# Performance work log

Measured on AMD Instinct MI355X. Metric: run time of the kernel, lower is better.

Reference implementation:

```python
import jax, jax.numpy as jnp
import numpy as np
from jax import lax

DG = 8  # deformable groups


def conv3(x, w, b):
    # 3x3 stride-1 SAME conv, NCHW/OIHW
    y = lax.conv_general_dilated(x, w, (1, 1), 'SAME',
                                 dimension_numbers=('NCHW', 'OIHW', 'NCHW'))
    return y + b[None, :, None, None]


def lrelu(x):
    return jnp.where(x >= 0, x, 0.1 * x)


def _mdcn(x, offset, mask, w, b, dg):
    """Modulated deformable conv v2: 3x3, stride 1, pad 1, dilation 1, groups 1.
    offset: [B, 2*dg*9, H, W] (first dg*9 = y offsets, second dg*9 = x offsets),
    mask:   [B, dg*9, H, W] (already sigmoided)."""
    B, C, H, W = x.shape
    kk = 9
    Cg = C // dg
    off = offset.reshape(B, 2, dg, kk, H, W)
    oy, ox = off[:, 0], off[:, 1]            # [B, dg, kk, H, W]
    m = mask.reshape(B, dg, kk, H, W)
    ky = (jnp.arange(kk) // 3 - 1).astype(x.dtype).reshape(1, 1, kk, 1, 1)
    kx = (jnp.arange(kk) % 3 - 1).astype(x.dtype).reshape(1, 1, kk, 1, 1)
    hg = jnp.arange(H, dtype=x.dtype).reshape(1, 1, 1, H, 1)
    wg = jnp.arange(W, dtype=x.dtype).reshape(1, 1, 1, 1, W)
    py = hg + ky + oy                        # sampling positions (pad=1 cancels k-1 shift)
    px = wg + kx + ox
    y0 = jnp.floor(py)
    x0 = jnp.floor(px)
    wy = py - y0
    wx = px - x0
    xg = x.reshape(B, dg, Cg, H * W)
    acc = jnp.zeros((B, dg, Cg, kk, H, W), x.dtype)
    for dy, dx, wgt in ((0.0, 0.0, (1 - wy) * (1 - wx)),
                        (0.0, 1.0, (1 - wy) * wx),
                        (1.0, 0.0, wy * (1 - wx)),
                        (1.0, 1.0, wy * wx)):
        yy = y0 + dy
        xx = x0 + dx
        valid = (yy >= 0) & (yy < H) & (xx >= 0) & (xx < W)
        yi = jnp.clip(yy, 0, H - 1).astype(jnp.int32)
        xi = jnp.clip(xx, 0, W - 1).astype(jnp.int32)
        idx = (yi * W + xi).reshape(B, dg, 1, kk * H * W)
        v = jnp.take_along_axis(xg, idx, axis=3).reshape(B, dg, Cg, kk, H, W)
        acc = acc + v * (wgt * valid.astype(x.dtype))[:, :, None]
    acc = acc * m[:, :, None]                # modulation mask
    sampled = acc.reshape(B, C, kk, H, W)
    out = jnp.einsum('bckhw,ock->bohw', sampled, w.reshape(w.shape[0], C, kk))
    return out + b[None, :, None, None]


def _dcn_pack(x, feat, w_om, b_om, w, b):
    out = conv3(feat, w_om, b_om)            # [B, 3*dg*9, H, W]
    o1, o2, mr = jnp.split(out, 3, axis=1)
    offset = jnp.concatenate([o1, o2], axis=1)
    mask = jax.nn.sigmoid(mr)
    return _mdcn(x, offset, mask, w, b, DG)


def _forward(ref, neb,
             w_oc1, b_oc1, w_om1, b_om1, w_dcn1, b_dcn1, w_fc, b_fc,
             w_cas1, b_cas1, w_cas2, b_cas2, w_om2, b_om2, w_dcn2, b_dcn2,
             w_ta1, b_ta1, w_ta2, b_ta2, w_ff, b_ff):
    start = ref
    # --- PCD alignment (nbr_feat_l = neb, ref_feat_l = ref) ---
    off = lrelu(conv3(jnp.concatenate([neb, ref], axis=1), w_oc1, b_oc1))
    feat = _dcn_pack(neb, off, w_om1, b_om1, w_dcn1, b_dcn1)
    feat = lrelu(conv3(feat, w_fc, b_fc))
    off = jnp.concatenate([feat, ref], axis=1)
    off = lrelu(conv3(lrelu(conv3(off, w_cas1, b_cas1)), w_cas2, b_cas2))
    feat = lrelu(_dcn_pack(feat, off, w_om2, b_om2, w_dcn2, b_dcn2))
    # --- TSA fusion (ref=ref, neb=feat) ---
    emb_ref = conv3(ref, w_ta1, b_ta1)
    emb = conv3(feat, w_ta2, b_ta2)
    corr = jnp.sum(emb * emb_ref, axis=1, keepdims=True)  # [B,1,H,W]
    feat = lrelu(conv3(ref * corr, w_ff, b_ff))
    return feat + start


def setup_inputs() -> dict:
    key = jax.random.key(0)
    ks = jax.random.split(key, 32)
    B, C, H, W = 4, 64, 180, 320
    s = 0.05
    p = lambda k, shape: (jax.random.normal(k, shape, jnp.float32) * s)
    OM = 3 * DG * 9  # 216
    return {
        'ref': jax.random.normal(ks[0], (B, C, H, W), jnp.float32),
        'neb': jax.random.normal(ks[1], (B, C, H, W), jnp.float32),
        'w_oc1': p(ks[2], (C, 2 * C, 3, 3)), 'b_oc1': p(ks[3], (C,)),
        'w_om1': p(ks[4], (OM, C, 3, 3)),    'b_om1': p(ks[5], (OM,)),
        'w_dcn1': p(ks[6], (C, C, 3, 3)),    'b_dcn1': p(ks[7], (C,)),
        'w_fc': p(ks[8], (C, C, 3, 3)),      'b_fc': p(ks[9], (C,)),
        'w_cas1': p(ks[10], (C, 2 * C, 3, 3)), 'b_cas1': p(ks[11], (C,)),
        'w_cas2': p(ks[12], (C, C, 3, 3)),   'b_cas2': p(ks[13], (C,)),
        'w_om2': p(ks[14], (OM, C, 3, 3)),   'b_om2': p(ks[15], (OM,)),
        'w_dcn2': p(ks[16], (C, C, 3, 3)),   'b_dcn2': p(ks[17], (C,)),
        'w_ta1': p(ks[18], (C, C, 3, 3)),    'b_ta1': p(ks[19], (C,)),
        'w_ta2': p(ks[20], (C, C, 3, 3)),    'b_ta2': p(ks[21], (C,)),
        'w_ff': p(ks[22], (C, C, 3, 3)),     'b_ff': p(ks[23], (C,)),
    }


def reference(ref, neb,
              w_oc1, b_oc1, w_om1, b_om1, w_dcn1, b_dcn1, w_fc, b_fc,
              w_cas1, b_cas1, w_cas2, b_cas2, w_om2, b_om2, w_dcn2, b_dcn2,
              w_ta1, b_ta1, w_ta2, b_ta2, w_ff, b_ff):
    return _forward(ref, neb,
                    w_oc1, b_oc1, w_om1, b_om1, w_dcn1, b_dcn1, w_fc, b_fc,
                    w_cas1, b_cas1, w_cas2, b_cas2, w_om2, b_om2, w_dcn2, b_dcn2,
                    w_ta1, b_ta1, w_ta2, b_ta2, w_ff, b_ff)
```

## Files before the change

kernel.cpp:

```cpp
#include <hip/hip_runtime.h>
#include <cmath>


using short8 = __attribute__((ext_vector_type(8))) short;
using f32x4  = __attribute__((ext_vector_type(4))) float;

#define DEVINL static __device__ __forceinline__

DEVINL unsigned short f2bf(float f){
    unsigned u = __float_as_uint(f);
    u += 0x7fffu + ((u >> 16) & 1u);
    return (unsigned short)(u >> 16);
}
DEVINL unsigned pack2(float a, float b){ return (unsigned)f2bf(a) | ((unsigned)f2bf(b) << 16); }
DEVINL float bflo(unsigned u){ return __uint_as_float(u << 16); }
DEVINL float bfhi(unsigned u){ return __uint_as_float(u & 0xffff0000u); }
DEVINL float bf2f(unsigned short u){ return __uint_as_float((unsigned)u << 16); }
DEVINL float lrelu_f(float v){ return v >= 0.f ? v : 0.1f * v; }

DEVINL void swz_decode(int& bx, int& by, int& bz){
    const int gx = gridDim.x, gy = gridDim.y;
    int lin = blockIdx.x + gx * (blockIdx.y + gy * blockIdx.z);
    int nwg = gx * gy * gridDim.z;
    int q = nwg >> 3, r = nwg & 7;
    int xcd = lin & 7, idx = lin >> 3;
    int swz = (xcd < r ? xcd * (q + 1) : r + xcd * q) + idx;
    bz = swz / (gx * gy);
    int rem = swz - bz * gx * gy;
    by = rem / gx; bx = rem - by * gx;
}

struct Ptr4 { unsigned short* p[4]; };

__global__ __launch_bounds__(256) void nchw2nhwc2(const float* __restrict__ inA,
                                                  const float* __restrict__ inB,
                                                  unsigned short* __restrict__ outA,
                                                  unsigned short* __restrict__ outB)
{
    constexpr int HW = 180 * 320;
    const int blk = blockIdx.x;
    const float* in = (blk < 900) ? inA : inB;
    unsigned short* out = (blk < 900) ? outA : outB;
    size_t idx = (size_t)(blk % 900) * 256 + threadIdx.x;
    size_t bb = idx / HW, p = idx % HW;
    const float* src = in + (bb * 64) * (size_t)HW + p;
    unsigned short* dst = out + idx * 64;
    #pragma unroll
    for (int c0 = 0; c0 < 64; c0 += 16) {
        unsigned r[8];
        #pragma unroll
        for (int q = 0; q < 8; ++q)
            r[q] = pack2(src[(size_t)(c0 + 2*q) * HW], src[(size_t)(c0 + 2*q + 1) * HW]);
        *(uint4*)(dst + c0)     = *(uint4*)&r[0];
        *(uint4*)(dst + c0 + 8) = *(uint4*)&r[4];
    }
}

struct PrepArgs {
    const float* src[11];
    unsigned short* dst[11];
    int cout[11]; int cin[11]; int nch[11]; int kind[11];
};

__global__ __launch_bounds__(256) void prep_all(PrepArgs a)
{
    const int t = blockIdx.y;
    const int idx = blockIdx.x * 256 + threadIdx.x;
    if (a.kind[t] == 1) {
        if (idx >= 36864) return;
        int kk = idx & 31, oc = (idx >> 5) & 63, s = idx >> 11;
        int k = s * 32 + kk;
        int gt = k >> 3, c8 = k & 7;
        int g = gt / 9, tp = gt - g * 9;
        a.dst[t][idx] = f2bf(a.src[t][((size_t)oc * 64 + g * 8 + c8) * 9 + tp]);
    } else {
        int cin = a.cin[t], cout = a.cout[t];
        int ncs = cin / 32;
        int total = a.nch[t] * 9 * ncs * 2048;
        if (idx >= total) return;
        int kk = idx & 31, oc_l = (idx >> 5) & 63, rest = idx >> 11;
        int cs = rest % ncs; int rest2 = rest / ncs;
        int j = rest2 % 9; int ch = rest2 / 9;
        int oc = ch * 64 + oc_l, c = cs * 32 + kk;
        float v = (oc < cout) ? a.src[t][((size_t)oc * cin + c) * 9 + j] : 0.f;
        a.dst[t][idx] = f2bf(v);
    }
}

template<int CIN, bool TWO_IN, bool ACT, bool SCALE, int OUTMODE, int NM>
__global__ __launch_bounds__(256, (CIN == 128 ? 2 : 3)) void conv_mfma(
    const unsigned short* __restrict__ in0, const unsigned short* __restrict__ in1,
    const unsigned short* __restrict__ wgt, const float* __restrict__ bias,
    unsigned short* __restrict__ out, const float* __restrict__ corr,
    const float* __restrict__ res, float* __restrict__ outf,
    Ptr4 omout, int choff, int zdiv, int COUT)
{
    constexpr int H = 180, W = 320, HW = H * W;
    constexpr int NCB = CIN / 8;
    constexpr int NCS = CIN / 32;
    __shared__ __align__(16) unsigned char lds[6 * 34 * CIN * 2];

    const int tid = threadIdx.x;
    int bx, by, bz;
    swz_decode(bx, by, bz);
    int b, ch;
    if (OUTMODE == 1) { b = bz / zdiv; ch = bz % zdiv + choff; }
    else              { b = bz; ch = 0; }
    const int x0 = bx * 32, y0 = by * 4;

    for (int t = tid; t < 6 * 34 * NCB; t += 256) {
        int cb = t % NCB; int r = t / NCB;
        int xp = r % 34, yp = r / 34;
        int gx = x0 - 1 + xp, gy = y0 - 1 + yp;
        uint4 v = make_uint4(0, 0, 0, 0);
        if (gx >= 0 && gx < W && gy >= 0 && gy < H) {
            size_t pix = (size_t)b * HW + (size_t)gy * W + gx;
            const unsigned short* src;
            if (TWO_IN) src = (cb < 8) ? (in0 + pix * 64 + cb * 8) : (in1 + pix * 64 + (cb - 8) * 8);
            else        src = in0 + pix * CIN + cb * 8;
            v = *(const uint4*)src;
            if (SCALE) {
                float cv = corr[pix];
                v.x = pack2(bflo(v.x) * cv, bfhi(v.x) * cv);
                v.y = pack2(bflo(v.y) * cv, bfhi(v.y) * cv);
                v.z = pack2(bflo(v.z) * cv, bfhi(v.z) * cv);
                v.w = pack2(bflo(v.w) * cv, bfhi(v.w) * cv);
            }
        }
        int blk = cb ^ (xp & 7);
        *(uint4*)&lds[(size_t)((yp * 34 + xp) * NCB + blk) * 16] = v;
    }
    __syncthreads();

    const int wv = tid >> 6, lane = tid & 63;
    const int ll = lane & 15, lh = lane >> 4;
    const unsigned short* wchunk = wgt + (size_t)ch * (9 * NCS * 2048);
    const int alane = ll * 32 + lh * 8;

    f32x4 acc[NM][2];
    #pragma unroll
    for (int mi = 0; mi < NM; ++mi)
        #pragma unroll
        for (int nf = 0; nf < 2; ++nf) acc[mi][nf] = f32x4{0.f, 0.f, 0.f, 0.f};

    #pragma unroll
    for (int j = 0; j < 9; ++j) {
        const int jy = j / 3, jx = j % 3;
        #pragma unroll
        for (int cs = 0; cs < NCS; ++cs) {
            const int s = j * NCS + cs;
            short8 a[NM];
            #pragma unroll
            for (int mi = 0; mi < NM; ++mi)
                a[mi] = *(const short8*)(wchunk + (size_t)s * 2048 + mi * 512 + alane);
            short8 bf[2];
            #pragma unroll
            for (int nf = 0; nf < 2; ++nf) {
                int xp = nf * 16 + ll + jx;
                int blk = (cs * 4 + lh) ^ (xp & 7);
                int addr = (((wv + jy) * 34 + xp) * NCB + blk) * 16;
                bf[nf] = *(const short8*)&lds[addr];
            }
            #pragma unroll
            for (int mi = 0; mi < NM; ++mi)
                #pragma unroll
                for (int nf = 0; nf < 2; ++nf)
                    acc[mi][nf] = __builtin_amdgcn_mfma_f32_16x16x32_bf16(a[mi], bf[nf], acc[mi][nf], 0, 0, 0);
        }
    }

    const int py = y0 + wv;
    const size_t pixrow = (size_t)b * HW + (size_t)py * W;
    #pragma unroll
    for (int nf = 0; nf < 2; ++nf) {
        const int px = x0 + nf * 16 + ll;
        if (OUTMODE == 3) {
            float dot = 0.f;
            const unsigned* er = (const unsigned*)(in1 + (pixrow + px) * 64);
            #pragma unroll
            for (int mi = 0; mi < NM; ++mi) {
                const int oc_l = mi * 16 + lh * 4;
                unsigned e0 = er[oc_l / 2], e1 = er[oc_l / 2 + 1];
                float t0 = acc[mi][nf][0] + bias[oc_l + 0];
                float t1 = acc[mi][nf][1] + bias[oc_l + 1];
                float t2 = acc[mi][nf][2] + bias[oc_l + 2];
                float t3 = acc[mi][nf][3] + bias[oc_l + 3];
                dot += t0 * bflo(e0) + t1 * bfhi(e0) + t2 * bflo(e1) + t3 * bfhi(e1);
            }
            dot += __shfl_xor(dot, 16);
            dot += __shfl_xor(dot, 32);
            if (lh == 0) outf[pixrow + px] = dot;
        } else if (OUTMODE == 1) {
            unsigned short* oslot = omout.p[b];
            #pragma unroll
            for (int mi = 0; mi < NM; ++mi) {
                const int oc_l = mi * 16 + lh * 4;
                #pragma unroll
                for (int jj = 0; jj < 4; ++jj) {
                    int ocg = ch * 64 + oc_l + jj;
                    if (ocg < COUT) {
                        float t = acc[mi][nf][jj] + bias[ocg];
                        oslot[(size_t)ocg * HW + (size_t)py * W + px] = f2bf(ACT ? lrelu_f(t) : t);
                    }
                }
            }
        } else {
            #pragma unroll
            for (int mi = 0; mi < NM; ++mi) {
                const int oc_l = mi * 16 + lh * 4;
                if (OUTMODE == 0) {
                    float v[4];
                    #pragma unroll
                    for (int jj = 0; jj < 4; ++jj) {
                        float t = acc[mi][nf][jj] + bias[oc_l + jj];
                        v[jj] = ACT ? lrelu_f(t) : t;
                    }
                    uint2 st; st.x = pack2(v[0], v[1]); st.y = pack2(v[2], v[3]);
                    *(uint2*)&out[(pixrow + px) * 64 + oc_l] = st;
                } else {
                    #pragma unroll
                    for (int jj = 0; jj < 4; ++jj) {
                        int oc = oc_l + jj;
                        float t = acc[mi][nf][jj] + bias[oc];
                        if (ACT) t = lrelu_f(t);
                        size_t idx = ((size_t)b * 64 + oc) * HW + (size_t)py * W + px;
                        outf[idx] = t + res[idx];
                    }
                }
            }
        }
    }
}

template<int ACT>
__global__ __launch_bounds__(256, 4) void mdcn_mfma(
    const unsigned short* __restrict__ x, size_t xstride,
    const unsigned short* __restrict__ om, size_t omstride,
    const unsigned short* __restrict__ wgt, const float* __restrict__ bias,
    unsigned short* __restrict__ out, size_t ostride)
{
    constexpr int H = 180, W = 320, HW = H * W;
    __shared__ __align__(16) unsigned char sv[72 * 32 * 16];

    const int tid = threadIdx.x;
    int bx, by, bz;
    swz_decode(bx, by, bz);
    const unsigned short* xb  = x  + (size_t)bz * xstride;
    const unsigned short* omb = om + (size_t)bz * omstride;
    unsigned short* ob        = out + (size_t)bz * ostride;
    const int px0 = bx * 32;
    const int py  = by;

    {
        const int pxl = tid & 31, g = tid >> 5;
        const int px = px0 + pxl;
        const size_t p = (size_t)py * W + px;
        const unsigned short* omg = omb + (size_t)(g * 9) * HW + p;

        float oyv[9], oxv[9], mmv[9];
        #pragma unroll
        for (int k = 0; k < 9; ++k) oyv[k] = bf2f(omg[(size_t)k * HW]);
        #pragma unroll
        for (int k = 0; k < 9; ++k) oxv[k] = bf2f(omg[(size_t)(72 + k) * HW]);
        #pragma unroll
        for (int k = 0; k < 9; ++k) mmv[k] = bf2f(omg[(size_t)(144 + k) * HW]);

        #pragma unroll
        for (int k = 0; k < 9; ++k) {
            float m = 1.f / (1.f + __expf(-mmv[k]));
            float pyf = (float)(py + (k / 3) - 1) + oyv[k];
            float pxf = (float)(px + (k % 3) - 1) + oxv[k];
            float y0f = floorf(pyf), x0f = floorf(pxf);
            float wy = pyf - y0f, wx = pxf - x0f;
            int yi = (int)y0f, xi = (int)x0f;
            bool vy0 = (yi >= 0) && (yi < H);
            bool vy1 = (yi + 1 >= 0) && (yi + 1 < H);
            bool vx0 = (xi >= 0) && (xi < W);
            bool vx1 = (xi + 1 >= 0) && (xi + 1 < W);
            float w00 = (vy0 && vx0) ? (1.f - wy) * (1.f - wx) * m : 0.f;
            float w01 = (vy0 && vx1) ? (1.f - wy) * wx * m : 0.f;
            float w10 = (vy1 && vx0) ? wy * (1.f - wx) * m : 0.f;
            float w11 = (vy1 && vx1) ? wy * wx * m : 0.f;
            int yc0 = min(max(yi, 0), H - 1), yc1 = min(max(yi + 1, 0), H - 1);
            int xc0 = min(max(xi, 0), W - 1), xc1 = min(max(xi + 1, 0), W - 1);
            uint4 c00 = *(const uint4*)(xb + ((size_t)(yc0 * W + xc0) * 64 + g * 8));
            uint4 c01 = *(const uint4*)(xb + ((size_t)(yc0 * W + xc1) * 64 + g * 8));
            uint4 c10 = *(const uint4*)(xb + ((size_t)(yc1 * W + xc0) * 64 + g * 8));
            uint4 c11 = *(const uint4*)(xb + ((size_t)(yc1 * W + xc1) * 64 + g * 8));
            const unsigned* p00 = (const unsigned*)&c00;
            const unsigned* p01 = (const unsigned*)&c01;
            const unsigned* p10 = (const unsigned*)&c10;
            const unsigned* p11 = (const unsigned*)&c11;
            unsigned r[4];
            #pragma unroll
            for (int q = 0; q < 4; ++q) {
                float lo = w00 * bflo(p00[q]) + w01 * bflo(p01[q]) + w10 * bflo(p10[q]) + w11 * bflo(p11[q]);
                float hi = w00 * bfhi(p00[q]) + w01 * bfhi(p01[q]) + w10 * bfhi(p10[q]) + w11 * bfhi(p11[q]);
                r[q] = pack2(lo, hi);
            }
            *(uint4*)&sv[(size_t)((g * 9 + k) * 32 + pxl) * 16] = *(uint4*)r;
        }
    }
    __syncthreads();

    const int wv = tid >> 6, lane = tid & 63;
    const int ll = lane & 15, lh = lane >> 4;
    f32x4 acc[2] = {f32x4{0.f,0.f,0.f,0.f}, f32x4{0.f,0.f,0.f,0.f}};
    #pragma unroll
    for (int s = 0; s < 18; ++s) {
        short8 a = *(const short8*)(wgt + (size_t)(s * 64 + wv * 16 + ll) * 32 + lh * 8);
        #pragma unroll
        for (int nf = 0; nf < 2; ++nf) {
            short8 bb = *(const short8*)&sv[(size_t)s * 2048 + lh * 512 + (nf * 16 + ll) * 16];
            acc[nf] = __builtin_amdgcn_mfma_f32_16x16x32_bf16(a, bb, acc[nf], 0, 0, 0);
        }
    }
    #pragma unroll
    for (int nf = 0; nf < 2; ++nf) {
        int opx = px0 + nf * 16 + ll;
        int oc0 = wv * 16 + lh * 4;
        float v[4];
        #pragma unroll
        for (int jj = 0; jj < 4; ++jj) {
            float t = acc[nf][jj] + bias[oc0 + jj];
            v[jj] = ACT ? lrelu_f(t) : t;
        }
        uint2 st; st.x = pack2(v[0], v[1]); st.y = pack2(v[2], v[3]);
        *(uint2*)&ob[((size_t)py * W + opx) * 64 + oc0] = st;
    }
}

extern "C" void kernel_launch(void* const* d_in, const int* in_sizes, int n_in,
                              void* d_out, int out_size, void* d_ws, size_t ws_size,
                              hipStream_t stream)
{
    const float* ref    = (const float*)d_in[0];
    const float* neb    = (const float*)d_in[1];
    const float* w_oc1  = (const float*)d_in[2];  const float* b_oc1  = (const float*)d_in[3];
    const float* w_om1  = (const float*)d_in[4];  const float* b_om1  = (const float*)d_in[5];
    const float* w_dcn1 = (const float*)d_in[6];  const float* b_dcn1 = (const float*)d_in[7];
    const float* w_fc   = (const float*)d_in[8];  const float* b_fc   = (const float*)d_in[9];
    const float* w_cas1 = (const float*)d_in[10]; const float* b_cas1 = (const float*)d_in[11];
    const float* w_cas2 = (const float*)d_in[12]; const float* b_cas2 = (const float*)d_in[13];
    const float* w_om2  = (const float*)d_in[14]; const float* b_om2  = (const float*)d_in[15];
    const float* w_dcn2 = (const float*)d_in[16]; const float* b_dcn2 = (const float*)d_in[17];
    const float* w_ta1  = (const float*)d_in[18]; const float* b_ta1  = (const float*)d_in[19];
    const float* w_ta2  = (const float*)d_in[20]; const float* b_ta2  = (const float*)d_in[21];
    const float* w_ff   = (const float*)d_in[22]; const float* b_ff   = (const float*)d_in[23];

    constexpr int H = 180, W = 320, HW = H * W;
    constexpr size_t CHW = (size_t)HW * 64;
    constexpr size_t SLB = 4 * CHW * 2;
    constexpr size_t OMSLOT_EL = (size_t)HW * 216;
    constexpr size_t OMSLOT_B  = OMSLOT_EL * 2;

    char* wsb = (char*)d_ws;
    unsigned short* S0 = (unsigned short*)(wsb);
    unsigned short* S1 = (unsigned short*)(wsb + SLB);
    unsigned short* S2 = (unsigned short*)(wsb + 2 * SLB);
    unsigned short* S3 = (unsigned short*)(wsb + 3 * SLB);
    float* corrf = (float*)S3;
    unsigned short* ffw = (unsigned short*)(wsb + SLB + (2u << 20));

    char* doutb = (char*)d_out;
    unsigned short* omA0 = (unsigned short*)doutb;
    unsigned short* omA1 = omA0 + OMSLOT_EL;
    unsigned short* wb   = (unsigned short*)(doutb + 2 * OMSLOT_B);
    const bool big = ws_size >= 4 * SLB + 2 * OMSLOT_B;
    unsigned short* omB0 = (unsigned short*)(wsb + 4 * SLB);
    unsigned short* omB1 = omB0 + OMSLOT_EL;

    unsigned short* w_oc1p = wb + 0;
    unsigned short* w_om1p = wb + 73728;
    unsigned short* w_dcn1p= wb + 221184;
    unsigned short* w_fcp  = wb + 258048;
    unsigned short* w_cas1p= wb + 294912;
    unsigned short* w_cas2p= wb + 368640;
    unsigned short* w_om2p = wb + 405504;
    unsigned short* w_dcn2p= wb + 552960;
    unsigned short* w_ta1p = wb + 589824;
    unsigned short* w_ta2p = wb + 626688;
    unsigned short* w_ffp  = wb + 663552;

    dim3 blk(256);
    dim3 g4(10, 45, 4);
    dim3 gm(10, 180, 2);
    Ptr4 none{};

    nchw2nhwc2<<<1800, blk, 0, stream>>>(ref, neb, S0, S1);

    {
        PrepArgs pa;
        const float* srcs[11] = {w_oc1, w_om1, w_dcn1, w_fc, w_cas1, w_cas2, w_om2, w_dcn2, w_ta1, w_ta2, w_ff};
        unsigned short* dsts[11] = {w_oc1p, w_om1p, w_dcn1p, w_fcp, w_cas1p, w_cas2p, w_om2p, w_dcn2p, w_ta1p, w_ta2p, w_ffp};
        int couts[11] = {64, 216, 0, 64, 64, 64, 216, 0, 64, 64, 64};
        int cins[11]  = {128, 64, 0, 64, 128, 64, 64, 0, 64, 64, 64};
        int nchs[11]  = {1, 4, 0, 1, 1, 1, 4, 0, 1, 1, 1};
        int kinds[11] = {0, 0, 1, 0, 0, 0, 0, 1, 0, 0, 0};
        for (int i = 0; i < 11; ++i) {
            pa.src[i] = srcs[i]; pa.dst[i] = dsts[i];
            pa.cout[i] = couts[i]; pa.cin[i] = cins[i]; pa.nch[i] = nchs[i]; pa.kind[i] = kinds[i];
        }
        prep_all<<<dim3(576, 11), blk, 0, stream>>>(pa);
    }

    conv_mfma<128, true, true, false, 0, 4><<<g4, blk, 0, stream>>>(
        S1, S0, w_oc1p, b_oc1, S2, nullptr, nullptr, nullptr, none, 0, 1, 64);

    auto ompack = [&](const unsigned short* inp, const unsigned short* wp, const float* bp,
                      Ptr4 slots, int nb){
        conv_mfma<64, false, false, false, 1, 4><<<dim3(10, 45, 3 * nb), blk, 0, stream>>>(
            inp, nullptr, wp, bp, nullptr, nullptr, nullptr, nullptr, slots, 0, 3, 216);
        conv_mfma<64, false, false, false, 1, 2><<<dim3(10, 45, nb), blk, 0, stream>>>(
            inp, nullptr, wp, bp, nullptr, nullptr, nullptr, nullptr, slots, 3, 1, 216);
    };

    if (big) {
        Ptr4 slots{omA0, omA1, omB0, omB1};
        ompack(S2, w_om1p, b_om1, slots, 4);
        mdcn_mfma<0><<<gm, blk, 0, stream>>>(S1, CHW, omA0, OMSLOT_EL, w_dcn1p, b_dcn1, S3, CHW);
        mdcn_mfma<0><<<gm, blk, 0, stream>>>(S1 + 2 * CHW, CHW, omB0, OMSLOT_EL, w_dcn1p, b_dcn1, S3 + 2 * CHW, CHW);
    } else {
        Ptr4 slots{omA0, omA1, nullptr, nullptr};
        for (int pp = 0; pp < 2; ++pp) {
            ompack(S2 + 2 * pp * CHW, w_om1p, b_om1, slots, 2);
            mdcn_mfma<0><<<gm, blk, 0, stream>>>(S1 + 2 * pp * CHW, CHW, omA0, OMSLOT_EL,
                                                 w_dcn1p, b_dcn1, S3 + 2 * pp * CHW, CHW);
        }
    }

    conv_mfma<64, false, true, false, 0, 4><<<g4, blk, 0, stream>>>(
        S3, nullptr, w_fcp, b_fc, S2, nullptr, nullptr, nullptr, none, 0, 1, 64);
    conv_mfma<128, true, true, false, 0, 4><<<g4, blk, 0, stream>>>(
        S2, S0, w_cas1p, b_cas1, S1, nullptr, nullptr, nullptr, none, 0, 1, 64);
    conv_mfma<64, false, true, false, 0, 4><<<g4, blk, 0, stream>>>(
        S1, nullptr, w_cas2p, b_cas2, S3, nullptr, nullptr, nullptr, none, 0, 1, 64);

    if (big) {
        Ptr4 slots{omA0, omA1, omB0, omB1};
        ompack(S3, w_om2p, b_om2, slots, 4);
        mdcn_mfma<1><<<gm, blk, 0, stream>>>(S2, CHW, omA0, OMSLOT_EL, w_dcn2p, b_dcn2, S1, CHW);
        mdcn_mfma<1><<<gm, blk, 0, stream>>>(S2 + 2 * CHW, CHW, omB0, OMSLOT_EL, w_dcn2p, b_dcn2, S1 + 2 * CHW, CHW);
    } else {
        Ptr4 slots{omA0, omA1, nullptr, nullptr};
        for (int pp = 0; pp < 2; ++pp) {
            ompack(S3 + 2 * pp * CHW, w_om2p, b_om2, slots, 2);
            mdcn_mfma<1><<<gm, blk, 0, stream>>>(S2 + 2 * pp * CHW, CHW, omA0, OMSLOT_EL,
                                                 w_dcn2p, b_dcn2, S1 + 2 * pp * CHW, CHW);
        }
    }

    conv_mfma<64, false, false, false, 0, 4><<<g4, blk, 0, stream>>>(
        S0, nullptr, w_ta1p, b_ta1, S2, nullptr, nullptr, nullptr, none, 0, 1, 64);
    conv_mfma<64, false, false, false, 3, 4><<<g4, blk, 0, stream>>>(
        S1, S2, w_ta2p, b_ta2, nullptr, nullptr, nullptr, corrf, none, 0, 1, 64);

    hipMemcpyAsync(ffw, w_ffp, 36864 * 2, hipMemcpyDeviceToDevice, stream);

    conv_mfma<64, false, true, true, 2, 4><<<g4, blk, 0, stream>>>(
        S0, nullptr, ffw, b_ff, nullptr, corrf, ref, (float*)d_out, none, 0, 1, 64);
}
```

Before: 1.185 ms.

## Add double-buffered async-LDS conv kernel for 64-channel 3x3 convolutions

Adds a new conv64_pipe kernel in which each block processes five 4-row tiles. It double-buffers the input halo in LDS using global_load_lds direct copies with an XOR swizzle, so the load of the next tile overlaps the MFMA work on the current one. Out-of-bounds halo elements are loaded from a zero buffer that the transpose kernel initialises. The grid shrinks so each block reuses its setup across tiles. This replaces the 64-input-channel conv launches (offset/mask convs, fc, cas2, ta1, ta2) and trades lower occupancy (launch bounds 3) and more LDS for overlap of memory and compute.

New measurement: 2.635 ms. 122% more time.

```diff
diff --git a/kernel.cpp b/kernel.cpp
--- a/kernel.cpp
+++ b/kernel.cpp
@@ -17,6 +17,12 @@
 DEVINL float bfhi(unsigned u){ return __uint_as_float(u & 0xffff0000u); }
 DEVINL float bf2f(unsigned short u){ return __uint_as_float((unsigned)u << 16); }
 DEVINL float lrelu_f(float v){ return v >= 0.f ? v : 0.1f * v; }
+
+typedef __attribute__((address_space(1))) const unsigned glob_u32;
+typedef __attribute__((address_space(3))) unsigned lds_u32;
+DEVINL void gload16(const void* g, void* l){
+    __builtin_amdgcn_global_load_lds((glob_u32*)g, (lds_u32*)l, 16, 0, 0);
+}
 
 DEVINL void swz_decode(int& bx, int& by, int& bz){
     const int gx = gridDim.x, gy = gridDim.y;
@@ -35,9 +41,11 @@
 __global__ __launch_bounds__(256) void nchw2nhwc2(const float* __restrict__ inA,
                                                   const float* __restrict__ inB,
                                                   unsigned short* __restrict__ outA,
-                                                  unsigned short* __restrict__ outB)
+                                                  unsigned short* __restrict__ outB,
+                                                  unsigned short* __restrict__ zp)
 {
     constexpr int HW = 180 * 320;
+    if (blockIdx.x == 0 && threadIdx.x == 0) *(uint4*)zp = make_uint4(0, 0, 0, 0);
     const int blk = blockIdx.x;
     const float* in = (blk < 900) ? inA : inB;
     unsigned short* out = (blk < 900) ? outA : outB;
@@ -229,6 +237,159 @@
                 }
             }
         }
+    }
+}
+
+template<bool ACT, int OUTMODE, int NM>
+__global__ __launch_bounds__(256, 3) void conv64_pipe(
+    const unsigned short* __restrict__ in0, const unsigned short* __restrict__ in1,
+    const unsigned short* __restrict__ wgt, const float* __restrict__ bias,
+    unsigned short* __restrict__ out, float* __restrict__ outf,
+    Ptr4 omout, int choff, int zdiv, const unsigned short* __restrict__ zp)
+{
+    constexpr int H = 180, W = 320, HW = H * W;
+    constexpr int NT = 5;
+    constexpr int NELEM = 6 * 34 * 8;
+    constexpr int NI = 26;
+    __shared__ __align__(16) unsigned short halo[2][1664 * 8];
+
+    const int tid = threadIdx.x;
+    const int wv = tid >> 6, lane = tid & 63;
+    int bx, by, bz;
+    swz_decode(bx, by, bz);
+    int b, ch;
+    if (OUTMODE == 1) { b = bz / zdiv; ch = bz % zdiv + choff; }
+    else              { b = bz; ch = 0; }
+    const int x0 = bx * 32;
+    const int yb0 = by * (NT * 4);
+
+    const unsigned short* inb = in0 + (size_t)b * HW * 64;
+
+    const unsigned short* srcx[7];
+    int ypk[7];
+    bool okx[7];
+    #pragma unroll
+    for (int k = 0; k < 7; ++k) {
+        int i = wv + 4 * k;
+        int e = i * 64 + lane;
+        int yp = e / 272, r = e - yp * 272;
+        int xp = r >> 3, cb = r & 7;
+        int cbs = cb ^ (xp & 7);
+        int gx = x0 - 1 + xp;
+        ypk[k] = yp;
+        okx[k] = (i < NI) && (e < NELEM) && (gx >= 0) && (gx < W);
+        srcx[k] = inb + (size_t)gx * 64 + cbs * 8;
+    }
+
+    auto stage = [&](int t, int bb){
+        int gyb = yb0 + t * 4 - 1;
+        #pragma unroll
+        for (int k = 0; k < 7; ++k) {
+            int i = wv + 4 * k;
+            if (i >= NI) break;
+            int gy = gyb + ypk[k];
+            const unsigned short* src = (okx[k] && gy >= 0 && gy < H)
+                                      ? srcx[k] + (size_t)gy * (W * 64) : zp;
+            gload16(src, &halo[bb][i * 512]);
+        }
+    };
+
+    const int ll = lane & 15, lh = lane >> 4;
+    const unsigned short* wchunk = wgt + (size_t)ch * (9 * 2 * 2048);
+    const int alane = ll * 32 + lh * 8;
+
+    stage(0, 0);
+    __syncthreads();
+
+    int buf = 0;
+    for (int t = 0; t < NT; ++t) {
+        if (t + 1 < NT) stage(t + 1, buf ^ 1);
+
+        const unsigned char* lds = (const unsigned char*)halo[buf];
+        f32x4 acc[NM][2];
+        #pragma unroll
+        for (int mi = 0; mi < NM; ++mi)
+            #pragma unroll
+            for (int nf = 0; nf < 2; ++nf) acc[mi][nf] = f32x4{0.f, 0.f, 0.f, 0.f};
+
+        #pragma unroll
+        for (int j = 0; j < 9; ++j) {
+            const int jy = j / 3, jx = j % 3;
+            #pragma unroll
+            for (int cs = 0; cs < 2; ++cs) {
+                const int s = j * 2 + cs;
+                short8 a[NM];
+                #pragma unroll
+                for (int mi = 0; mi < NM; ++mi)
+                    a[mi] = *(const short8*)(wchunk + (size_t)s * 2048 + mi * 512 + alane);
+                short8 bf[2];
+                #pragma unroll
+                for (int nf = 0; nf < 2; ++nf) {
+                    int xp = nf * 16 + ll + jx;
+                    int blk = (cs * 4 + lh) ^ (xp & 7);
+                    int addr = (((wv + jy) * 34 + xp) * 8 + blk) * 16;
+                    bf[nf] = *(const short8*)&lds[addr];
+                }
+                #pragma unroll
+                for (int mi = 0; mi < NM; ++mi)
+                    #pragma unroll
+                    for (int nf = 0; nf < 2; ++nf)
+                        acc[mi][nf] = __builtin_amdgcn_mfma_f32_16x16x32_bf16(a[mi], bf[nf], acc[mi][nf], 0, 0, 0);
+            }
+        }
+
+        const int py = yb0 + t * 4 + wv;
+        const size_t pixrow = (size_t)b * HW + (size_t)py * W;
+        #pragma unroll
+        for (int nf = 0; nf < 2; ++nf) {
+            const int px = x0 + nf * 16 + ll;
+            if (OUTMODE == 3) {
+                float dot = 0.f;
+                const unsigned* er = (const unsigned*)(in1 + (pixrow + px) * 64);
+                #pragma unroll
+                for (int mi = 0; mi < NM; ++mi) {
+                    const int oc_l = mi * 16 + lh * 4;
+                    unsigned e0 = er[oc_l / 2], e1 = er[oc_l / 2 + 1];
+                    float t0 = acc[mi][nf][0] + bias[oc_l + 0];
+                    float t1 = acc[mi][nf][1] + bias[oc_l + 1];
+                    float t2 = acc[mi][nf][2] + bias[oc_l + 2];
+                    float t3 = acc[mi][nf][3] + bias[oc_l + 3];
+                    dot += t0 * bflo(e0) + t1 * bfhi(e0) + t2 * bflo(e1) + t3 * bfhi(e1);
+                }
+                dot += __shfl_xor(dot, 16);
+                dot += __shfl_xor(dot, 32);
+                if (lh == 0) outf[pixrow + px] = dot;
+            } else if (OUTMODE == 1) {
+                unsigned short* oslot = omout.p[b];
+                #pragma unroll
+                for (int mi = 0; mi < NM; ++mi) {
+                    const int oc_l = mi * 16 + lh * 4;
+                    #pragma unroll
+                    for (int jj = 0; jj < 4; ++jj) {
+                        int ocg = ch * 64 + oc_l + jj;
+                        if (ocg < 216) {
+                            float tv = acc[mi][nf][jj] + bias[ocg];
+                            oslot[(size_t)ocg * HW + (size_t)py * W + px] = f2bf(ACT ? lrelu_f(tv) : tv);
+                        }
+                    }
+                }
+            } else {
+                #pragma unroll
+                for (int mi = 0; mi < NM; ++mi) {
+                    const int oc_l = mi * 16 + lh * 4;
+                    float v[4];
+                    #pragma unroll
+                    for (int jj = 0; jj < 4; ++jj) {
+                        float tv = acc[mi][nf][jj] + bias[oc_l + jj];
+                        v[jj] = ACT ? lrelu_f(tv) : tv;
+                    }
+                    uint2 st; st.x = pack2(v[0], v[1]); st.y = pack2(v[2], v[3]);
+                    *(uint2*)&out[(pixrow + px) * 64 + oc_l] = st;
+                }
+            }
+        }
+        __syncthreads();
+        buf ^= 1;
     }
 }
 
@@ -366,6 +527,7 @@
     unsigned short* omA0 = (unsigned short*)doutb;
     unsigned short* omA1 = omA0 + OMSLOT_EL;
     unsigned short* wb   = (unsigned short*)(doutb + 2 * OMSLOT_B);
+    unsigned short* zp   = (unsigned short*)(doutb + 56u * 1024 * 1024);
     const bool big = ws_size >= 4 * SLB + 2 * OMSLOT_B;
     unsigned short* omB0 = (unsigned short*)(wsb + 4 * SLB);
     unsigned short* omB1 = omB0 + OMSLOT_EL;
@@ -383,11 +545,12 @@
     unsigned short* w_ffp  = wb + 663552;
 
     dim3 blk(256);
+    dim3 gp(10, 9, 4);
     dim3 g4(10, 45, 4);
     dim3 gm(10, 180, 2);
     Ptr4 none{};
 
-    nchw2nhwc2<<<1800, blk, 0, stream>>>(ref, neb, S0, S1);
+    nchw2nhwc2<<<1800, blk, 0, stream>>>(ref, neb, S0, S1, zp);
 
     {
         PrepArgs pa;
@@ -409,10 +572,10 @@
 
     auto ompack = [&](const unsigned short* inp, const unsigned short* wp, const float* bp,
                       Ptr4 slots, int nb){
-        conv_mfma<64, false, false, false, 1, 4><<<dim3(10, 45, 3 * nb), blk, 0, stream>>>(
-            inp, nullptr, wp, bp, nullptr, nullptr, nullptr, nullptr, slots, 0, 3, 216);
-        conv_mfma<64, false, false, false, 1, 2><<<dim3(10, 45, nb), blk, 0, stream>>>(
-            inp, nullptr, wp, bp, nullptr, nullptr, nullptr, nullptr, slots, 3, 1, 216);
+        conv64_pipe<false, 1, 4><<<dim3(10, 9, 3 * nb), blk, 0, stream>>>(
+            inp, nullptr, wp, bp, nullptr, nullptr, slots, 0, 3, zp);
+        conv64_pipe<false, 1, 2><<<dim3(10, 9, nb), blk, 0, stream>>>(
+            inp, nullptr, wp, bp, nullptr, nullptr, slots, 3, 1, zp);
     };
 
     if (big) {
@@ -429,12 +592,12 @@
         }
     }
 
-    conv_mfma<64, false, true, false, 0, 4><<<g4, blk, 0, stream>>>(
-        S3, nullptr, w_fcp, b_fc, S2, nullptr, nullptr, nullptr, none, 0, 1, 64);
+    conv64_pipe<true, 0, 4><<<gp, blk, 0, stream>>>(
+        S3, nullptr, w_fcp, b_fc, S2, nullptr, none, 0, 1, zp);
     conv_mfma<128, true, true, false, 0, 4><<<g4, blk, 0, stream>>>(
         S2, S0, w_cas1p, b_cas1, S1, nullptr, nullptr, nullptr, none, 0, 1, 64);
-    conv_mfma<64, false, true, false, 0, 4><<<g4, blk, 0, stream>>>(
-        S1, nullptr, w_cas2p, b_cas2, S3, nullptr, nullptr, nullptr, none, 0, 1, 64);
+    conv64_pipe<true, 0, 4><<<gp, blk, 0, stream>>>(
+        S1, nullptr, w_cas2p, b_cas2, S3, nullptr, none, 0, 1, zp);
 
     if (big) {
         Ptr4 slots{omA0, omA1, omB0, omB1};
@@ -450,10 +613,10 @@
         }
     }
 
-    conv_mfma<64, false, false, false, 0, 4><<<g4, blk, 0, stream>>>(
-        S0, nullptr, w_ta1p, b_ta1, S2, nullptr, nullptr, nullptr, none, 0, 1, 64);
-    conv_mfma<64, false, false, false, 3, 4><<<g4, blk, 0, stream>>>(
-        S1, S2, w_ta2p, b_ta2, nullptr, nullptr, nullptr, corrf, none, 0, 1, 64);
+    conv64_pipe<false, 0, 4><<<gp, blk, 0, stream>>>(
+        S0, nullptr, w_ta1p, b_ta1, S2, nullptr, none, 0, 1, zp);
+    conv64_pipe<false, 3, 4><<<gp, blk, 0, stream>>>(
+        S1, S2, w_ta2p, b_ta2, nullptr, corrf, none, 0, 1, zp);
 
     hipMemcpyAsync(ffw, w_ffp, 36864 * 2, hipMemcpyDeviceToDevice, stream);
 
```
